# Optimization experiments

Measured on AMD Instinct MI355X. Metric: run time of the kernel, lower is better.

## Reference

```python
import jax, jax.numpy as jnp
import numpy as np

N = 100000
E = 1600000
IN_C, HID_C, OUT_C = 128, 64, 16


def setup_inputs() -> dict:
    key = jax.random.key(0)
    k1, k2, k3, k4, k5 = jax.random.split(key, 5)
    x = jax.random.normal(k1, (N, IN_C), dtype=jnp.float32)
    edge_index = jax.random.randint(k2, (2, E), 0, N, dtype=jnp.int64)
    edge_weight = jax.random.uniform(k3, (E,), dtype=jnp.float32)
    # GCNConv weights (Glorot init, bias=False)
    W1 = jax.random.normal(k4, (IN_C, HID_C), dtype=jnp.float32) * (1.0 / np.sqrt(IN_C))
    W2 = jax.random.normal(k5, (HID_C, OUT_C), dtype=jnp.float32) * (1.0 / np.sqrt(HID_C))
    return {"x": x, "edge_index": edge_index, "edge_weight": edge_weight, "W1": W1, "W2": W2}


def _gcn_norm(edge_index, edge_weight, num_nodes):
    # add self loops with weight 1 (PyG gcn_norm with add_self_loops=True)
    loop = jnp.arange(num_nodes, dtype=edge_index.dtype)
    row = jnp.concatenate([edge_index[0], loop])
    col = jnpp_concat = jnp.concatenate([edge_index[1], loop])
    w = jnp.concatenate([edge_weight, jnp.ones((num_nodes,), edge_weight.dtype)])
    deg = jax.ops.segment_sum(w, col, num_segments=num_nodes)
    dinv = jnp.where(deg > 0, jax.lax.rsqrt(deg), 0.0)
    norm = dinv[row] * w * dinv[col]
    return row, col, norm


def _gcn_conv(x, W, row, col, norm, num_nodes):
    h = x @ W                              # [N, C_out] dense projection
    msg = h[row] * norm[:, None]           # gather + scale per edge
    return jax.ops.segment_sum(msg, col, num_segments=num_nodes)  # scatter-add at dst


def reference(x, edge_index, edge_weight, W1, W2):
    num_nodes = x.shape[0]
    row, col, norm = _gcn_norm(edge_index, edge_weight, num_nodes)
    h = _gcn_conv(x, W1, row, col, norm, num_nodes)
    h = jax.nn.relu(h)  # dropout_rate == 0 / eval -> identity
    h = _gcn_conv(h, W2, row, col, norm, num_nodes)
    return jax.nn.log_softmax(h, axis=1)
```

## Files before the change

kernel.cpp:

```cpp
#include <hip/hip_runtime.h>
#include <hip/hip_fp16.h>
#include <math.h>

constexpr int IN_C = 128, HID_C = 64, OUT_C = 16;
constexpr int BSH = 7;
constexpr int BCAP = 2560;
constexpr int REC_PT = BCAP / 256;
constexpr int TILE = 4096;
constexpr float WSC = 33554432.0f;

using f16x8 = __attribute__((ext_vector_type(8))) _Float16;
using f32x4 = __attribute__((ext_vector_type(4))) float;

__global__ __launch_bounds__(256) void k_hist(const int* __restrict__ col, int* __restrict__ histG,
                                              int E, int nb) {
  __shared__ int h[1024];
  int t = threadIdx.x, tile = blockIdx.x;
  for (int i = t; i < nb; i += 256) h[i] = 0;
  __syncthreads();
  int base = tile * TILE;
#pragma unroll
  for (int u = 0; u < TILE / 256; ++u) {
    int e = base + u * 256 + t;
    if (e < E) atomicAdd(&h[col[e] >> BSH], 1);
  }
  __syncthreads();
  for (int i = t; i < nb; i += 256) histG[(size_t)tile * nb + i] = h[i];
}

__global__ __launch_bounds__(256) void k_cscan(int* __restrict__ histG, int* __restrict__ btot,
                                               int T, int nb) {
  int b = blockIdx.x, t = threadIdx.x;
  __shared__ int s[512];
  int i0 = t, i1 = t + 256;
  s[i0] = (i0 < T) ? histG[(size_t)i0 * nb + b] : 0;
  s[i1] = (i1 < T) ? histG[(size_t)i1 * nb + b] : 0;
  __syncthreads();
  int c0 = s[i0], c1 = s[i1];
  for (int off = 1; off < 512; off <<= 1) {
    int a0 = (i0 >= off) ? s[i0 - off] : 0;
    int a1 = (i1 >= off) ? s[i1 - off] : 0;
    __syncthreads();
    s[i0] += a0; s[i1] += a1;
    __syncthreads();
  }
  if (i0 < T) histG[(size_t)i0 * nb + b] = s[i0] - c0;
  if (i1 < T) histG[(size_t)i1 * nb + b] = s[i1] - c1;
  if (t == 0) btot[b] = s[511];
}

__global__ __launch_bounds__(256) void k_scat2(const int* __restrict__ row, const int* __restrict__ col,
                                               const float* __restrict__ w, const int* __restrict__ histG,
                                               uint2* __restrict__ rec, int E, int nb) {
  __shared__ int soff[1024];
  int t = threadIdx.x, tile = blockIdx.x;
  for (int i = t; i < nb; i += 256) soff[i] = histG[(size_t)tile * nb + i];
  __syncthreads();
  int base = tile * TILE;
#pragma unroll
  for (int u = 0; u < TILE / 256; ++u) {
    int e = base + u * 256 + t;
    if (e < E) {
      int r = row[e], d = col[e];
      int b = d >> BSH;
      unsigned lo = (unsigned)(d & ((1 << BSH) - 1));
      unsigned wf = __float2uint_rn(w[e] * WSC);
      if (wf > 33554431u) wf = 33554431u;
      int slot = atomicAdd(&soff[b], 1);
      if (slot < BCAP)
        rec[(size_t)b * BCAP + slot] = make_uint2((unsigned)r, (lo << 25) | wf);
    }
  }
}

__global__ __launch_bounds__(256) void k_buck(const int* __restrict__ btot, const uint2* __restrict__ rec,
                                              int2* __restrict__ pairs, int* __restrict__ ptrg,
                                              int* __restrict__ cntg, float* __restrict__ dinvg,
                                              int n) {
  int b = blockIdx.x;
  int t = threadIdx.x;
  int cnt = btot[b];
  if (cnt > BCAP) cnt = BCAP;
  __shared__ int lcnt[128];
  __shared__ float lws[128];
  __shared__ int lptr[128];
  if (t < 128) { lcnt[t] = 0; lws[t] = 0.f; }
  __syncthreads();
  uint2 rv[REC_PT];
  int rk[REC_PT];
#pragma unroll
  for (int u = 0; u < REC_PT; ++u) {
    int i = u * 256 + t;
    if (i < cnt) {
      uint2 v = rec[(size_t)b * BCAP + i];
      rv[u] = v;
      int lo = v.y >> 25;
      rk[u] = atomicAdd(&lcnt[lo], 1);
      atomicAdd(&lws[lo], (float)(v.y & 0x1FFFFFFu) * (1.0f / WSC));
    }
  }
  __syncthreads();
  if (t < 128) lptr[t] = lcnt[t];
  __syncthreads();
  for (int off = 1; off < 128; off <<= 1) {
    int v = (t < 128 && t >= off) ? lptr[t - off] : 0;
    __syncthreads();
    if (t < 128 && t >= off) lptr[t] += v;
    __syncthreads();
  }
  if (t < 128) {
    int d = (b << BSH) + t;
    if (d < n) {
      ptrg[d] = b * BCAP + lptr[t] - lcnt[t];
      cntg[d] = lcnt[t];
      dinvg[d] = rsqrtf(1.0f + lws[t]);
    }
  }
#pragma unroll
  for (int u = 0; u < REC_PT; ++u) {
    int i = u * 256 + t;
    if (i < cnt) {
      uint2 v = rv[u];
      int lo = v.y >> 25;
      float wv = (float)(v.y & 0x1FFFFFFu) * (1.0f / WSC);
      pairs[(size_t)b * BCAP + (lptr[lo] - lcnt[lo]) + rk[u]] = make_int2((int)v.x, __float_as_int(wv));
    }
  }
}

__global__ __launch_bounds__(256) void k_gemm1(const float* __restrict__ x, const float* __restrict__ W1,
                                               const float* __restrict__ dinv,
                                               __half* __restrict__ h1h, int n) {
  __shared__ _Float16 w1t[HID_C][IN_C];
  int t = threadIdx.x;
  for (int i = t; i < IN_C * HID_C / 4; i += 256) {
    float4 v = ((const float4*)W1)[i];
    int k = (i * 4) / HID_C;
    int c = (i * 4) % HID_C;
    w1t[c + 0][k] = (_Float16)v.x;
    w1t[c + 1][k] = (_Float16)v.y;
    w1t[c + 2][k] = (_Float16)v.z;
    w1t[c + 3][k] = (_Float16)v.w;
  }
  __syncthreads();
  int wave = t >> 6, lane = t & 63;
  int row0 = (blockIdx.x * 4 + wave) * 16;
  if (row0 >= n) return;
  int lrow = lane & 15, lkg = lane >> 4;
  bool rvalid = (row0 + lrow) < n;
  const float* xr = x + (size_t)(row0 + lrow) * IN_C;
  f32x4 acc[4];
#pragma unroll
  for (int cg = 0; cg < 4; ++cg) acc[cg] = (f32x4){0.f, 0.f, 0.f, 0.f};
#pragma unroll
  for (int ks = 0; ks < 4; ++ks) {
    int k0 = ks * 32 + lkg * 8;
    f16x8 a;
    if (rvalid) {
      float4 u0 = *(const float4*)&xr[k0];
      float4 u1 = *(const float4*)&xr[k0 + 4];
      a[0] = (_Float16)u0.x; a[1] = (_Float16)u0.y; a[2] = (_Float16)u0.z; a[3] = (_Float16)u0.w;
      a[4] = (_Float16)u1.x; a[5] = (_Float16)u1.y; a[6] = (_Float16)u1.z; a[7] = (_Float16)u1.w;
    } else {
#pragma unroll
      for (int j = 0; j < 8; ++j) a[j] = (_Float16)0.f;
    }
#pragma unroll
    for (int cg = 0; cg < 4; ++cg) {
      f16x8 bfrag = *(const f16x8*)&w1t[cg * 16 + lrow][k0];
      acc[cg] = __builtin_amdgcn_mfma_f32_16x16x32_f16(a, bfrag, acc[cg], 0, 0, 0);
    }
  }
  float dv[4];
#pragma unroll
  for (int r = 0; r < 4; ++r) {
    int gr = row0 + lkg * 4 + r;
    dv[r] = (gr < n) ? dinv[gr] : 0.f;
  }
#pragma unroll
  for (int cg = 0; cg < 4; ++cg) {
#pragma unroll
    for (int r = 0; r < 4; ++r) {
      int gr = row0 + lkg * 4 + r;
      if (gr < n)
        h1h[(size_t)gr * HID_C + cg * 16 + lrow] = __float2half_rn(dv[r] * acc[cg][r]);
    }
  }
}

__global__ __launch_bounds__(256) void k_agg1f(const int* __restrict__ ptr, const int* __restrict__ cnt,
                                               const int2* __restrict__ pairs, const float* __restrict__ dinv,
                                               const __half* __restrict__ h1h, const float* __restrict__ W2,
                                               __half* __restrict__ h2h, int n) {
  __shared__ float w2s[HID_C * OUT_C];
  __shared__ float s[4][68];
  int t = threadIdx.x;
  ((float4*)w2s)[t] = ((const float4*)W2)[t];
  int wv = t >> 6, lane = t & 63;
  int d = blockIdx.x * 4 + wv;
  if (d < n) {
    d = __builtin_amdgcn_readfirstlane(d);
    int k = ptr[d], end = k + cnt[d];
    float dd = dinv[d];
    float acc = __half2float(h1h[(size_t)d * HID_C + lane]);
    for (; k + 8 <= end; k += 8) {
      int2 p[8];
      float v[8];
#pragma unroll
      for (int u = 0; u < 8; ++u) p[u] = pairs[k + u];
#pragma unroll
      for (int u = 0; u < 8; ++u)
        v[u] = __half2float(h1h[(size_t)p[u].x * HID_C + lane]);
#pragma unroll
      for (int u = 0; u < 8; ++u) acc = fmaf(__int_as_float(p[u].y), v[u], acc);
    }
    if (k + 4 <= end) {
      int2 p[4];
      float v[4];
#pragma unroll
      for (int u = 0; u < 4; ++u) p[u] = pairs[k + u];
#pragma unroll
      for (int u = 0; u < 4; ++u)
        v[u] = __half2float(h1h[(size_t)p[u].x * HID_C + lane]);
#pragma unroll
      for (int u = 0; u < 4; ++u) acc = fmaf(__int_as_float(p[u].y), v[u], acc);
      k += 4;
    }
    for (; k < end; ++k) {
      int2 p = pairs[k];
      acc = fmaf(__int_as_float(p.y), __half2float(h1h[(size_t)p.x * HID_C + lane]), acc);
    }
    s[wv][lane] = fmaxf(dd * acc, 0.f);
  } else {
    s[wv][lane] = 0.f;
  }
  __syncthreads();
  if (t < 64) {
    int nl = t >> 4, j = t & 15;
    int dn = blockIdx.x * 4 + nl;
    if (dn < n) {
      float a2 = 0.f;
#pragma unroll
      for (int c = 0; c < HID_C; ++c) a2 = fmaf(s[nl][c], w2s[c * OUT_C + j], a2);
      h2h[(size_t)dn * OUT_C + j] = __float2half_rn(dinv[dn] * a2);
    }
  }
}

__global__ __launch_bounds__(256) void k_agg2(const int* __restrict__ ptr, const int* __restrict__ cnt,
                                              const int2* __restrict__ pairs, const float* __restrict__ dinv,
                                              const __half* __restrict__ h2h, float* __restrict__ out, int n) {
  int t = threadIdx.x;
  int d = blockIdx.x * 16 + (t >> 4);
  if (d >= n) return;
  int j = t & 15;
  int k = ptr[d], end = k + cnt[d];
  float dd = dinv[d];
  float acc = __half2float(h2h[(size_t)d * OUT_C + j]);
  for (; k + 8 <= end; k += 8) {
    int2 p[8];
    float v[8];
#pragma unroll
    for (int u = 0; u < 8; ++u) p[u] = pairs[k + u];
#pragma unroll
    for (int u = 0; u < 8; ++u)
      v[u] = __half2float(h2h[(size_t)p[u].x * OUT_C + j]);
#pragma unroll
    for (int u = 0; u < 8; ++u) acc = fmaf(__int_as_float(p[u].y), v[u], acc);
  }
  if (k + 4 <= end) {
    int2 p[4];
    float v[4];
#pragma unroll
    for (int u = 0; u < 4; ++u) p[u] = pairs[k + u];
#pragma unroll
    for (int u = 0; u < 4; ++u)
      v[u] = __half2float(h2h[(size_t)p[u].x * OUT_C + j]);
#pragma unroll
    for (int u = 0; u < 4; ++u) acc = fmaf(__int_as_float(p[u].y), v[u], acc);
    k += 4;
  }
  for (; k < end; ++k) {
    int2 p = pairs[k];
    acc = fmaf(__int_as_float(p.y), __half2float(h2h[(size_t)p.x * OUT_C + j]), acc);
  }
  float lg = dd * acc;
  float mx = lg;
#pragma unroll
  for (int off = 8; off; off >>= 1) mx = fmaxf(mx, __shfl_xor(mx, off, 16));
  float sm = expf(lg - mx);
#pragma unroll
  for (int off = 8; off; off >>= 1) sm += __shfl_xor(sm, off, 16);
  out[(size_t)d * OUT_C + j] = lg - mx - logf(sm);
}

extern "C" void kernel_launch(void* const* d_in, const int* in_sizes, int n_in,
                              void* d_out, int out_size, void* d_ws, size_t ws_size,
                              hipStream_t stream) {
  const float* x  = (const float*)d_in[0];
  const int*   ei = (const int*)d_in[1];
  const float* ew = (const float*)d_in[2];
  const float* W1 = (const float*)d_in[3];
  const float* W2 = (const float*)d_in[4];
  const int N = in_sizes[0] / IN_C;
  const int E = in_sizes[2];
  const int* row = ei;
  const int* col = ei + E;
  float* out = (float*)d_out;
  const int NBUK = (N + (1 << BSH) - 1) >> BSH;
  const int T = (E + TILE - 1) / TILE;

  char* p = (char*)d_ws;
  int2*  pairs= (int2*)p;             p += (size_t)NBUK * BCAP * 8;
  int*   ptr  = (int*)p;              p += (size_t)N * 4;
  int*   cnt  = (int*)p;              p += (size_t)N * 4;
  float* dinv = (float*)p;            p += (size_t)N * 4;
  int*   histG= (int*)p;              p += (size_t)T * NBUK * 4;
  int*   btot = (int*)p;              p += (size_t)NBUK * 4;
  char*  uni  = p;                    p += (size_t)N * HID_C * 4;
  uint2* rec  = (uint2*)uni;
  __half* h1h = (__half*)uni;
  __half* h2h = (__half*)(uni + (size_t)N * HID_C * 2);

  dim3 b(256);
  k_hist <<<T, b, 0, stream>>>(col, histG, E, NBUK);
  k_cscan<<<NBUK, b, 0, stream>>>(histG, btot, T, NBUK);
  k_scat2<<<T, b, 0, stream>>>(row, col, ew, histG, rec, E, NBUK);
  k_buck <<<NBUK, b, 0, stream>>>(btot, rec, pairs, ptr, cnt, dinv, N);
  k_gemm1<<<(N + 63) / 64, b, 0, stream>>>(x, W1, dinv, h1h, N);
  k_agg1f<<<(N + 3) / 4, b, 0, stream>>>(ptr, cnt, pairs, dinv, h1h, W2, h2h, N);
  k_agg2 <<<(N + 15) / 16, b, 0, stream>>>(ptr, cnt, pairs, dinv, h2h, out, N);
}
```

Before: 162.1 us.

## Vectorize agg1 gathers, stage bucket pairs in LDS, use nontemporal edge loads

```diff
diff --git a/kernel.cpp b/kernel.cpp
--- a/kernel.cpp
+++ b/kernel.cpp
@@ -10,7 +10,23 @@
 constexpr float WSC = 33554432.0f;
 
 using f16x8 = __attribute__((ext_vector_type(8))) _Float16;
+using f16x4 = __attribute__((ext_vector_type(4))) _Float16;
 using f32x4 = __attribute__((ext_vector_type(4))) float;
+
+static __device__ inline int2 ldnt2(const int2* p) {
+  unsigned long long v = __builtin_nontemporal_load((const unsigned long long*)p);
+  int2 r; r.x = (int)(unsigned)(v & 0xffffffffull); r.y = (int)(unsigned)(v >> 32);
+  return r;
+}
+static __device__ inline uint2 ldnt2u(const uint2* p) {
+  unsigned long long v = __builtin_nontemporal_load((const unsigned long long*)p);
+  uint2 r; r.x = (unsigned)(v & 0xffffffffull); r.y = (unsigned)(v >> 32);
+  return r;
+}
+static __device__ inline void stnt2u(uint2* p, uint2 v) {
+  unsigned long long q = ((unsigned long long)v.y << 32) | v.x;
+  __builtin_nontemporal_store(q, (unsigned long long*)p);
+}
 
 __global__ __launch_bounds__(256) void k_hist(const int* __restrict__ col, int* __restrict__ histG,
                                               int E, int nb) {
@@ -68,7 +84,7 @@
       if (wf > 33554431u) wf = 33554431u;
       int slot = atomicAdd(&soff[b], 1);
       if (slot < BCAP)
-        rec[(size_t)b * BCAP + slot] = make_uint2((unsigned)r, (lo << 25) | wf);
+        stnt2u(&rec[(size_t)b * BCAP + slot], make_uint2((unsigned)r, (lo << 25) | wf));
     }
   }
 }
@@ -84,6 +100,7 @@
   __shared__ int lcnt[128];
   __shared__ float lws[128];
   __shared__ int lptr[128];
+  __shared__ int2 sp[BCAP];
   if (t < 128) { lcnt[t] = 0; lws[t] = 0.f; }
   __syncthreads();
   uint2 rv[REC_PT];
@@ -92,7 +109,7 @@
   for (int u = 0; u < REC_PT; ++u) {
     int i = u * 256 + t;
     if (i < cnt) {
-      uint2 v = rec[(size_t)b * BCAP + i];
+      uint2 v = ldnt2u(&rec[(size_t)b * BCAP + i]);
       rv[u] = v;
       int lo = v.y >> 25;
       rk[u] = atomicAdd(&lcnt[lo], 1);
@@ -123,9 +140,12 @@
       uint2 v = rv[u];
       int lo = v.y >> 25;
       float wv = (float)(v.y & 0x1FFFFFFu) * (1.0f / WSC);
-      pairs[(size_t)b * BCAP + (lptr[lo] - lcnt[lo]) + rk[u]] = make_int2((int)v.x, __float_as_int(wv));
-    }
-  }
+      sp[(lptr[lo] - lcnt[lo]) + rk[u]] = make_int2((int)v.x, __float_as_int(wv));
+    }
+  }
+  __syncthreads();
+  for (int i = t; i < cnt; i += 256)
+    pairs[(size_t)b * BCAP + i] = sp[i];
 }
 
 __global__ __launch_bounds__(256) void k_gemm1(const float* __restrict__ x, const float* __restrict__ W1,
@@ -193,46 +213,60 @@
                                                const __half* __restrict__ h1h, const float* __restrict__ W2,
                                                __half* __restrict__ h2h, int n) {
   __shared__ float w2s[HID_C * OUT_C];
-  __shared__ float s[4][68];
+  __shared__ __align__(16) float s[4][68];
   int t = threadIdx.x;
   ((float4*)w2s)[t] = ((const float4*)W2)[t];
+  __syncthreads();
   int wv = t >> 6, lane = t & 63;
+  int g = lane >> 4;
+  int c4 = (lane & 15) * 4;
   int d = blockIdx.x * 4 + wv;
   if (d < n) {
     d = __builtin_amdgcn_readfirstlane(d);
     int k = ptr[d], end = k + cnt[d];
     float dd = dinv[d];
-    float acc = __half2float(h1h[(size_t)d * HID_C + lane]);
-    for (; k + 8 <= end; k += 8) {
-      int2 p[8];
-      float v[8];
-#pragma unroll
-      for (int u = 0; u < 8; ++u) p[u] = pairs[k + u];
+    f32x4 acc = {0.f, 0.f, 0.f, 0.f};
+    if (g == 0) {
+      f16x4 sv = *(const f16x4*)&h1h[(size_t)d * HID_C + c4];
+      acc[0] = (float)sv[0]; acc[1] = (float)sv[1];
+      acc[2] = (float)sv[2]; acc[3] = (float)sv[3];
+    }
+    int last = end - 1;
+    for (; k < end; k += 32) {
+      int2 p[8]; float w[8]; f16x4 v[8];
+#pragma unroll
+      for (int u = 0; u < 8; ++u) {
+        int idx = k + u * 4 + g;
+        int ic = (idx <= last) ? idx : last;
+        p[u] = ldnt2(&pairs[ic]);
+        w[u] = (idx <= last) ? __int_as_float(p[u].y) : 0.f;
+      }
 #pragma unroll
       for (int u = 0; u < 8; ++u)
-        v[u] = __half2float(h1h[(size_t)p[u].x * HID_C + lane]);
-#pragma unroll
-      for (int u = 0; u < 8; ++u) acc = fmaf(__int_as_float(p[u].y), v[u], acc);
-    }
-    if (k + 4 <= end) {
-      int2 p[4];
-      float v[4];
-#pragma unroll
-      for (int u = 0; u < 4; ++u) p[u] = pairs[k + u];
-#pragma unroll
-      for (int u = 0; u < 4; ++u)
-        v[u] = __half2float(h1h[(size_t)p[u].x * HID_C + lane]);
-#pragma unroll
-      for (int u = 0; u < 4; ++u) acc = fmaf(__int_as_float(p[u].y), v[u], acc);
-      k += 4;
-    }
-    for (; k < end; ++k) {
-      int2 p = pairs[k];
-      acc = fmaf(__int_as_float(p.y), __half2float(h1h[(size_t)p.x * HID_C + lane]), acc);
-    }
-    s[wv][lane] = fmaxf(dd * acc, 0.f);
+        v[u] = *(const f16x4*)&h1h[(size_t)p[u].x * HID_C + c4];
+#pragma unroll
+      for (int u = 0; u < 8; ++u) {
+        acc[0] = fmaf(w[u], (float)v[u][0], acc[0]);
+        acc[1] = fmaf(w[u], (float)v[u][1], acc[1]);
+        acc[2] = fmaf(w[u], (float)v[u][2], acc[2]);
+        acc[3] = fmaf(w[u], (float)v[u][3], acc[3]);
+      }
+    }
+#pragma unroll
+    for (int i = 0; i < 4; ++i) {
+      acc[i] += __shfl_xor(acc[i], 16);
+      acc[i] += __shfl_xor(acc[i], 32);
+    }
+    if (g == 0) {
+      float4 r;
+      r.x = fmaxf(dd * acc[0], 0.f);
+      r.y = fmaxf(dd * acc[1], 0.f);
+      r.z = fmaxf(dd * acc[2], 0.f);
+      r.w = fmaxf(dd * acc[3], 0.f);
+      *(float4*)&s[wv][c4] = r;
+    }
   } else {
-    s[wv][lane] = 0.f;
+    if (g == 0) *(float4*)&s[wv][c4] = make_float4(0.f, 0.f, 0.f, 0.f);
   }
   __syncthreads();
   if (t < 64) {
@@ -261,7 +295,7 @@
     int2 p[8];
     float v[8];
 #pragma unroll
-    for (int u = 0; u < 8; ++u) p[u] = pairs[k + u];
+    for (int u = 0; u < 8; ++u) p[u] = ldnt2(&pairs[k + u]);
 #pragma unroll
     for (int u = 0; u < 8; ++u)
       v[u] = __half2float(h2h[(size_t)p[u].x * OUT_C + j]);
@@ -272,7 +306,7 @@
     int2 p[4];
     float v[4];
 #pragma unroll
-    for (int u = 0; u < 4; ++u) p[u] = pairs[k + u];
+    for (int u = 0; u < 4; ++u) p[u] = ldnt2(&pairs[k + u]);
 #pragma unroll
     for (int u = 0; u < 4; ++u)
       v[u] = __half2float(h2h[(size_t)p[u].x * OUT_C + j]);
@@ -281,7 +315,7 @@
     k += 4;
   }
   for (; k < end; ++k) {
-    int2 p = pairs[k];
+    int2 p = ldnt2(&pairs[k]);
     acc = fmaf(__int_as_float(p.y), __half2float(h2h[(size_t)p.x * OUT_C + j]), acc);
   }
   float lg = dd * acc;
```

Result: slower. 192.9 us (+19.0%).
